# Kernel optimization log

Measured on AMD Instinct MI355X. Metric: run time of the kernel, lower is better.

The kernel has to match this reference:

```python
import jax, jax.numpy as jnp
import numpy as np

NFFT = 512
HOP = 256
N_FREQ = NFFT // 2


def _imdct_kernels():
    # Matches _get_imdct_kernels: windowed IMDCT cosine basis, shape [nfft, nfft//2]
    def kernel_fn(time, freq):
        win = np.sin(np.pi * (2 * time + 1) / (2.0 * NFFT))
        return np.cos(np.pi / NFFT * (2 * time + 1 + NFFT / 2.0) * (freq + 0.5)) * win
    k = np.fromfunction(kernel_fn, (NFFT, N_FREQ), dtype=np.float64)
    return jnp.asarray(k.astype(np.float32))  # [nfft, n_freq]


def setup_inputs() -> dict:
    key = jax.random.key(0)
    spec = jax.random.normal(key, (16, 1, N_FREQ, 4096), dtype=jnp.float32)
    return {"spec": spec, "kernels": _imdct_kernels()}


def reference(spec, kernels):
    # spec: [B, 1, n_freq, T]; kernels: [nfft, n_freq]
    B, _, _, T = spec.shape
    # conv2d with (n_freq,1) kernel == per-frame basis matmul over frequency
    frames = jnp.einsum('bft,kf->btk', spec[:, 0], kernels) * (4.0 / NFFT)  # [B, T, nfft]
    # conv_transpose2d with identity-diagonal kernel and stride=hop == overlap-add
    L = (T - 1) * HOP + NFFT
    idx = jnp.arange(T)[:, None] * HOP + jnp.arange(NFFT)[None, :]  # [T, nfft]
    out = jnp.zeros((B, L), dtype=spec.dtype).at[:, idx].add(frames)
    return out
```

## Files before the change

### kernel.cpp

```cpp
#include <hip/hip_runtime.h>
#include <stdint.h>

#define NFREQ 256
#define NB 16
#define NT 4096
#define LOUT 1048832
#define TROWS 33
#define TROW 132

typedef __bf16 bf16;
typedef __bf16 bf16x8 __attribute__((ext_vector_type(8)));
typedef float floatx4 __attribute__((ext_vector_type(4)));

__device__ inline uint32_t f_as_u(float x) { union { float f; uint32_t u; } v; v.f = x; return v.u; }
__device__ inline uint32_t bf16r(float x) {
    uint32_t u = f_as_u(x);
    return (u + 0x7fffu + ((u >> 16) & 1u)) >> 16;
}

__global__ __launch_bounds__(256) void build_kb(const float* __restrict__ ker,
                                                bf16* __restrict__ kbF) {
    int idx = blockIdx.x * 256 + threadIdx.x;
    int n = idx >> 9, f = idx & 511;
    float v = (f < 256) ? ker[(n + 256) * 256 + f] : ker[n * 256 + (f - 256)];
    uint32_t rr = bf16r(v * 0.0078125f);
    union { uint16_t u; bf16 b; } o; o.u = (uint16_t)rr;
    kbF[((size_t)(f >> 5) * 256 + n) * 32 + (f & 31)] = o.b;
}

__global__ __launch_bounds__(256, 6) void imdct_gemm(const float* __restrict__ spec,
                                                     const bf16* __restrict__ kbF,
                                                     float* __restrict__ out) {
    __shared__ uint32_t Tt[TROWS * TROW];

    const int jt = blockIdx.x;
    const int b  = blockIdx.y;
    const int tid = threadIdx.x, lane = tid & 63, w = tid >> 6;
    const int j0 = jt * 32;
    const float* sb = spec + (size_t)b * NFREQ * NT;

    {
        const int lpar = lane & 1, lt = lane >> 1;
        const int fpw = w * 32;
        const int t = j0 - 1 + lt;
        const bool tok = ((unsigned)t < (unsigned)NT);
        #pragma unroll
        for (int rb = 0; rb < 2; ++rb) {
            float v[16];
            #pragma unroll
            for (int i = 0; i < 16; ++i) {
                int fpi = rb * 16 + i;
                int f = (fpw + fpi) * 2 + lpar;
                v[i] = tok ? sb[(size_t)f * NT + t] : 0.0f;
            }
            #pragma unroll
            for (int i = 0; i < 16; i += 4) {
                uint32_t pk[4];
                #pragma unroll
                for (int u = 0; u < 4; ++u) {
                    uint32_t h = bf16r(v[i + u]);
                    uint32_t o = (uint32_t)__shfl_xor((int)h, 1);
                    pk[u] = (h & 0xffffu) | (o << 16);
                }
                if (lpar == 0) {
                    uint4 q4; q4.x = pk[0]; q4.y = pk[1]; q4.z = pk[2]; q4.w = pk[3];
                    *reinterpret_cast<uint4*>(&Tt[lt * TROW + fpw + rb * 16 + i]) = q4;
                }
            }
        }
        {
            int f = w * 64 + lane;
            int te = j0 + 31;
            float v = ((unsigned)te < (unsigned)NT) ? sb[(size_t)f * NT + te] : 0.0f;
            uint32_t h = bf16r(v); uint32_t o = (uint32_t)__shfl_xor((int)h, 1);
            if (lpar == 0) Tt[32 * TROW + w * 32 + lt] = (h & 0xffffu) | (o << 16);
        }
    }
    __syncthreads();

    const int row16 = lane & 15, q = lane >> 4;
    floatx4 acc[2][4] = {};
    const uint8_t* Tb = reinterpret_cast<const uint8_t*>(Tt);
    const bf16* kbw = kbF + (size_t)w * 64 * 32;

    for (int kki = 0; kki < 8; ++kki) {
        const int toff = (kki >= 4) ? 1 : 0;
        const int kbyte = (kki & 3) * 128;
        #pragma unroll
        for (int ks = 0; ks < 2; ++ks) {
            const int kchunk = kki * 2 + ks;
            bf16x8 af[2], bfr[4];
            #pragma unroll
            for (int i = 0; i < 2; ++i)
                af[i] = *reinterpret_cast<const bf16x8*>(
                    Tb + (size_t)(i * 16 + row16 + toff) * (TROW * 4) + kbyte + ks * 64 + q * 16);
            #pragma unroll
            for (int jn = 0; jn < 4; ++jn)
                bfr[jn] = *reinterpret_cast<const bf16x8*>(
                    kbw + (size_t)kchunk * 8192 + (jn * 16 + row16) * 32 + q * 8);
            #pragma unroll
            for (int i = 0; i < 2; ++i)
                #pragma unroll
                for (int jn = 0; jn < 4; ++jn)
                    acc[i][jn] = __builtin_amdgcn_mfma_f32_16x16x32_bf16(af[i], bfr[jn], acc[i][jn], 0, 0, 0);
        }
    }

    #pragma unroll
    for (int i = 0; i < 2; ++i) {
        #pragma unroll
        for (int e = 0; e < 4; ++e) {
            int j = j0 + i * 16 + q * 4 + e;
            if (j <= 4096) {
                float* orow = out + (size_t)b * LOUT + (size_t)j * 256 + w * 64;
                #pragma unroll
                for (int jn = 0; jn < 4; ++jn)
                    orow[jn * 16 + row16] = acc[i][jn][e];
            }
        }
    }
}

extern "C" void kernel_launch(void* const* d_in, const int* in_sizes, int n_in,
                              void* d_out, int out_size, void* d_ws, size_t ws_size,
                              hipStream_t stream) {
    const float* spec = (const float*)d_in[0];
    const float* ker  = (const float*)d_in[1];
    float* out = (float*)d_out;

    bf16* kbF = (bf16*)d_ws;

    build_kb<<<512, 256, 0, stream>>>(ker, kbF);
    imdct_gemm<<<dim3(129, NB), 256, 0, stream>>>(spec, kbF, out);
}
```

Baseline: 152.8 us.

## Enlarge time tile to 128 frames per block and double-buffer B fragments

Result: faster. 145.1 us (-5.1%).

```diff
diff --git a/kernel.cpp b/kernel.cpp
--- a/kernel.cpp
+++ b/kernel.cpp
@@ -5,7 +5,7 @@
 #define NB 16
 #define NT 4096
 #define LOUT 1048832
-#define TROWS 33
+#define TROWS 129
 #define TROW 132
 
 typedef __bf16 bf16;
@@ -28,7 +28,7 @@
     kbF[((size_t)(f >> 5) * 256 + n) * 32 + (f & 31)] = o.b;
 }
 
-__global__ __launch_bounds__(256, 6) void imdct_gemm(const float* __restrict__ spec,
+__global__ __launch_bounds__(256, 2) void imdct_gemm(const float* __restrict__ spec,
                                                      const bf16* __restrict__ kbF,
                                                      float* __restrict__ out) {
     __shared__ uint32_t Tt[TROWS * TROW];
@@ -36,25 +36,28 @@
     const int jt = blockIdx.x;
     const int b  = blockIdx.y;
     const int tid = threadIdx.x, lane = tid & 63, w = tid >> 6;
-    const int j0 = jt * 32;
+    const int j0 = jt * 128;
     const float* sb = spec + (size_t)b * NFREQ * NT;
 
     {
         const int lpar = lane & 1, lt = lane >> 1;
         const int fpw = w * 32;
-        const int t = j0 - 1 + lt;
-        const bool tok = ((unsigned)t < (unsigned)NT);
         #pragma unroll
-        for (int rb = 0; rb < 2; ++rb) {
+        for (int rb = 0; rb < 8; ++rb) {
             float v[16];
             #pragma unroll
             for (int i = 0; i < 16; ++i) {
-                int fpi = rb * 16 + i;
+                int r = rb * 16 + i;
+                int tc = r >> 5, fpi = r & 31;
                 int f = (fpw + fpi) * 2 + lpar;
-                v[i] = tok ? sb[(size_t)f * NT + t] : 0.0f;
+                int t = j0 - 1 + tc * 32 + lt;
+                v[i] = ((unsigned)t < (unsigned)NT) ? sb[(size_t)f * NT + t] : 0.0f;
             }
             #pragma unroll
             for (int i = 0; i < 16; i += 4) {
+                int r = rb * 16 + i;
+                int tc = r >> 5, fpi = r & 31;
+                int tl = tc * 32 + lt;
                 uint32_t pk[4];
                 #pragma unroll
                 for (int u = 0; u < 4; ++u) {
@@ -64,50 +67,61 @@
                 }
                 if (lpar == 0) {
                     uint4 q4; q4.x = pk[0]; q4.y = pk[1]; q4.z = pk[2]; q4.w = pk[3];
-                    *reinterpret_cast<uint4*>(&Tt[lt * TROW + fpw + rb * 16 + i]) = q4;
+                    *reinterpret_cast<uint4*>(&Tt[tl * TROW + fpw + fpi]) = q4;
                 }
             }
         }
         {
             int f = w * 64 + lane;
-            int te = j0 + 31;
+            int te = j0 + 127;
             float v = ((unsigned)te < (unsigned)NT) ? sb[(size_t)f * NT + te] : 0.0f;
             uint32_t h = bf16r(v); uint32_t o = (uint32_t)__shfl_xor((int)h, 1);
-            if (lpar == 0) Tt[32 * TROW + w * 32 + lt] = (h & 0xffffu) | (o << 16);
+            if (lpar == 0) Tt[128 * TROW + w * 32 + lt] = (h & 0xffffu) | (o << 16);
         }
     }
     __syncthreads();
 
     const int row16 = lane & 15, q = lane >> 4;
-    floatx4 acc[2][4] = {};
+    floatx4 acc[8][4] = {};
     const uint8_t* Tb = reinterpret_cast<const uint8_t*>(Tt);
     const bf16* kbw = kbF + (size_t)w * 64 * 32;
 
-    for (int kki = 0; kki < 8; ++kki) {
-        const int toff = (kki >= 4) ? 1 : 0;
-        const int kbyte = (kki & 3) * 128;
-        #pragma unroll
-        for (int ks = 0; ks < 2; ++ks) {
-            const int kchunk = kki * 2 + ks;
-            bf16x8 af[2], bfr[4];
-            #pragma unroll
-            for (int i = 0; i < 2; ++i)
-                af[i] = *reinterpret_cast<const bf16x8*>(
-                    Tb + (size_t)(i * 16 + row16 + toff) * (TROW * 4) + kbyte + ks * 64 + q * 16);
-            #pragma unroll
-            for (int jn = 0; jn < 4; ++jn)
-                bfr[jn] = *reinterpret_cast<const bf16x8*>(
-                    kbw + (size_t)kchunk * 8192 + (jn * 16 + row16) * 32 + q * 8);
-            #pragma unroll
-            for (int i = 0; i < 2; ++i)
-                #pragma unroll
-                for (int jn = 0; jn < 4; ++jn)
-                    acc[i][jn] = __builtin_amdgcn_mfma_f32_16x16x32_bf16(af[i], bfr[jn], acc[i][jn], 0, 0, 0);
-        }
+#define LOADB(dst, c) { \
+    _Pragma("unroll") \
+    for (int jn = 0; jn < 4; ++jn) \
+        dst[jn] = *reinterpret_cast<const bf16x8*>( \
+            kbw + (size_t)(c) * 8192 + (jn * 16 + row16) * 32 + q * 8); }
+
+#define LOADA(dst, c) { \
+    _Pragma("unroll") \
+    for (int i = 0; i < 8; ++i) \
+        dst[i] = *reinterpret_cast<const bf16x8*>( \
+            Tb + (size_t)(i * 16 + row16 + ((c) >> 3)) * 528 + ((c) & 7) * 64 + q * 16); }
+
+#define DOMFMA(afr, bfr) { \
+    _Pragma("unroll") \
+    for (int i = 0; i < 8; ++i) \
+        _Pragma("unroll") \
+        for (int jn = 0; jn < 4; ++jn) \
+            acc[i][jn] = __builtin_amdgcn_mfma_f32_16x16x32_bf16(afr[i], bfr[jn], acc[i][jn], 0, 0, 0); }
+
+    bf16x8 bP[4], bQ[4], af[8];
+    LOADB(bP, 0);
+    #pragma unroll
+    for (int cc = 0; cc < 8; ++cc) {
+        LOADB(bQ, cc * 2 + 1);
+        LOADA(af, cc * 2);
+        DOMFMA(af, bP);
+        if (cc < 7) LOADB(bP, cc * 2 + 2);
+        LOADA(af, cc * 2 + 1);
+        DOMFMA(af, bQ);
     }
+#undef LOADB
+#undef LOADA
+#undef DOMFMA
 
     #pragma unroll
-    for (int i = 0; i < 2; ++i) {
+    for (int i = 0; i < 8; ++i) {
         #pragma unroll
         for (int e = 0; e < 4; ++e) {
             int j = j0 + i * 16 + q * 4 + e;
@@ -131,5 +145,5 @@
     bf16* kbF = (bf16*)d_ws;
 
     build_kb<<<512, 256, 0, stream>>>(ker, kbF);
-    imdct_gemm<<<dim3(129, NB), 256, 0, stream>>>(spec, kbF, out);
+    imdct_gemm<<<dim3(33, NB), 256, 0, stream>>>(spec, kbF, out);
 }
```
